# Performance work log

Measured on AMD Instinct MI355X. Metric: run time of the kernel, lower is better.

## Reference

```python
import jax, jax.numpy as jnp
import numpy as np

B, C, H, W = 32, 512, 32, 32
C8 = C // 8


def setup_inputs() -> dict:
    key = jax.random.key(0)
    ks = jax.random.split(key, 10)
    s = 1.0 / np.sqrt(C)
    return {
        "x": jax.random.normal(ks[0], (B, C, H, W), dtype=jnp.float32),
        "hha": jax.random.normal(ks[1], (B, C, H, W), dtype=jnp.float32),
        "wq": jax.random.normal(ks[2], (C8, C), dtype=jnp.float32) * s,
        "bq": jax.random.normal(ks[3], (C8,), dtype=jnp.float32) * 0.01,
        "wk": jax.random.normal(ks[4], (C8, C), dtype=jnp.float32) * s,
        "bk": jax.random.normal(ks[5], (C8,), dtype=jnp.float32) * 0.01,
        "wv": jax.random.normal(ks[6], (C, C), dtype=jnp.float32) * s,
        "bv": jax.random.normal(ks[7], (C,), dtype=jnp.float32) * 0.01,
        "gamma": jax.random.normal(ks[8], (1,), dtype=jnp.float32) * 0.5,
    }


def reference(x, hha, wq, bq, wk, bk, wv, bv, gamma):
    b, c, h, w = x.shape
    hw = h * w
    # 1x1 convs == per-pixel channel matmuls
    q = (jnp.einsum('bchw,oc->bohw', x, wq) + bq[None, :, None, None]).reshape(b, -1, hw)
    k = (jnp.einsum('bchw,oc->bohw', x, wk) + bk[None, :, None, None]).reshape(b, -1, hw)
    v = (jnp.einsum('bchw,oc->bohw', x, wv) + bv[None, :, None, None]).reshape(b, c, hw)
    # energy[b, i, j] = q[b, :, i] . k[b, :, j]  (no 1/sqrt(d) scaling, as in source)
    energy = jnp.einsum('bci,bcj->bij', q, k)          # [B, HW, HW]
    attention = jax.nn.softmax(energy, axis=-1)
    # out = V @ attention^T : out[b, c, i] = sum_j v[b, c, j] * attention[b, i, j]
    out = jnp.einsum('bcj,bij->bci', v, attention).reshape(b, c, h, w)
    rgb_out = gamma * out + x
    hha_out = gamma * out + hha
    return (attention, rgb_out, hha_out)
```

## Files before the change

### kernel.cpp

```cpp
#include <hip/hip_runtime.h>

#define B_N   32
#define C_N   512
#define HW_N  1024
#define C8_N  64

typedef short bf16x8 __attribute__((ext_vector_type(8)));
typedef float f32x4  __attribute__((ext_vector_type(4)));

static __device__ __forceinline__ unsigned int bf16_bits(float a)
{
    unsigned int u = __float_as_uint(a);
    return (u + 0x7fffu + ((u >> 16) & 1u)) >> 16;
}

static __device__ __forceinline__ unsigned int pack2_bf16(float a, float b)
{
    return bf16_bits(a) | (bf16_bits(b) << 16);
}

__global__ __launch_bounds__(256) void xsplit_transpose_kernel(
    const float* __restrict__ x, unsigned int* __restrict__ xt)
{
    const int b   = blockIdx.z;
    const int c0  = blockIdx.y * 64;
    const int p0  = blockIdx.x * 64;
    const int tid = threadIdx.x;

    __shared__ unsigned int Ls[64][65];

    const float* xb = x + ((size_t)b * C_N + c0) * HW_N + p0;
    {
        const int c = tid >> 4;
        const int p = (tid & 15) * 4;
        #pragma unroll
        for (int s = 0; s < 4; ++s) {
            const float4 t = *(const float4*)(xb + (size_t)(c + 16 * s) * HW_N + p);
            const float v[4] = { t.x, t.y, t.z, t.w };
            #pragma unroll
            for (int j = 0; j < 4; ++j) {
                const unsigned int hi = bf16_bits(v[j]);
                const float hif = __uint_as_float(hi << 16);
                const unsigned int lo = bf16_bits(v[j] - hif);
                Ls[c + 16 * s][p + j] = (hi << 16) | lo;
            }
        }
    }
    __syncthreads();
    unsigned int* xo = xt + ((size_t)b * HW_N + p0) * C_N + c0;
    {
        const int p = tid >> 4;
        const int c = (tid & 15) * 4;
        #pragma unroll
        for (int s = 0; s < 4; ++s) {
            uint4 r;
            r.x = Ls[c + 0][p + 16 * s];
            r.y = Ls[c + 1][p + 16 * s];
            r.z = Ls[c + 2][p + 16 * s];
            r.w = Ls[c + 3][p + 16 * s];
            *(uint4*)(xo + (size_t)(p + 16 * s) * C_N + c) = r;
        }
    }
}

__global__ __launch_bounds__(256) void qkv_mfma_kernel(
    const unsigned int* __restrict__ xt,
    const float* __restrict__ wq, const float* __restrict__ bq,
    const float* __restrict__ wk, const float* __restrict__ bk,
    const float* __restrict__ wv, const float* __restrict__ bv,
    float* __restrict__ qk, unsigned short* __restrict__ vout)
{
    const int b    = blockIdx.z;
    const int by   = blockIdx.y;
    const int p0   = blockIdx.x * 128;
    const int tid  = threadIdx.x;
    const bool qkblk = (by == 0);

    __shared__ __align__(16) unsigned short AsHi[128 * 64];
    __shared__ __align__(16) unsigned short AsLo[128 * 64];
    __shared__ __align__(16) unsigned short BsHi[128 * 64];
    __shared__ __align__(16) unsigned short BsLo[128 * 64];

    const int sq = tid & 7;
    const int sr = tid >> 3;

    const int lane = tid & 63;
    const int wave = tid >> 6;
    const int wrow = (wave >> 1) * 64;
    const int wcol = (wave & 1) * 64;
    const int lrow = lane & 15;
    const int lk   = lane >> 4;

    const unsigned int* bt = xt + ((size_t)b * HW_N + p0) * C_N;

    f32x4 acc[4][4] = {};
    float4 ra[4][2];
    uint4  rb[4][2];

    auto wrowptr = [&](int r) -> const float* {
        if (qkblk) return (r < 64) ? (wq + (size_t)r * C_N)
                                   : (wk + (size_t)(r - 64) * C_N);
        return wv + (size_t)((by - 1) * 128 + r) * C_N;
    };

    auto load_tiles = [&](int k0) {
        #pragma unroll
        for (int s = 0; s < 4; ++s) {
            const int r = sr + 32 * s;
            const float* pa = wrowptr(r) + k0 + sq * 8;
            ra[s][0] = *(const float4*)(pa);
            ra[s][1] = *(const float4*)(pa + 4);
            const unsigned int* pb = bt + (size_t)r * C_N + k0 + sq * 8;
            rb[s][0] = *(const uint4*)(pb);
            rb[s][1] = *(const uint4*)(pb + 4);
        }
    };

    auto write_tiles = [&]() {
        #pragma unroll
        for (int s = 0; s < 4; ++s) {
            const int r  = sr + 32 * s;
            const int ch = sq ^ (r & 7);
            const float e[8] = { ra[s][0].x, ra[s][0].y, ra[s][0].z, ra[s][0].w,
                                 ra[s][1].x, ra[s][1].y, ra[s][1].z, ra[s][1].w };
            unsigned int h[8];
            #pragma unroll
            for (int j = 0; j < 8; ++j) h[j] = bf16_bits(e[j]);
            uint4 ah;
            ah.x = h[0] | (h[1] << 16); ah.y = h[2] | (h[3] << 16);
            ah.z = h[4] | (h[5] << 16); ah.w = h[6] | (h[7] << 16);
            *reinterpret_cast<uint4*>(&AsHi[r * 64 + ch * 8]) = ah;
            if (qkblk) {
                unsigned int l[8];
                #pragma unroll
                for (int j = 0; j < 8; ++j) {
                    const float hf = __uint_as_float(h[j] << 16);
                    l[j] = bf16_bits(e[j] - hf);
                }
                uint4 al;
                al.x = l[0] | (l[1] << 16); al.y = l[2] | (l[3] << 16);
                al.z = l[4] | (l[5] << 16); al.w = l[6] | (l[7] << 16);
                *reinterpret_cast<uint4*>(&AsLo[r * 64 + ch * 8]) = al;
            }
            const unsigned int q0[8] = { rb[s][0].x, rb[s][0].y, rb[s][0].z, rb[s][0].w,
                                         rb[s][1].x, rb[s][1].y, rb[s][1].z, rb[s][1].w };
            uint4 bh, bl;
            bh.x = (q0[0] >> 16) | (q0[1] & 0xffff0000u);
            bh.y = (q0[2] >> 16) | (q0[3] & 0xffff0000u);
            bh.z = (q0[4] >> 16) | (q0[5] & 0xffff0000u);
            bh.w = (q0[6] >> 16) | (q0[7] & 0xffff0000u);
            bl.x = (q0[0] & 0xffffu) | (q0[1] << 16);
            bl.y = (q0[2] & 0xffffu) | (q0[3] << 16);
            bl.z = (q0[4] & 0xffffu) | (q0[5] << 16);
            bl.w = (q0[6] & 0xffffu) | (q0[7] << 16);
            *reinterpret_cast<uint4*>(&BsHi[r * 64 + ch * 8]) = bh;
            *reinterpret_cast<uint4*>(&BsLo[r * 64 + ch * 8]) = bl;
        }
    };

    load_tiles(0);
    for (int kt = 0; kt < C_N / 64; ++kt) {
        __syncthreads();
        write_tiles();
        __syncthreads();
        if (kt + 1 < C_N / 64) load_tiles((kt + 1) * 64);

        #pragma unroll
        for (int kb = 0; kb < 2; ++kb) {
            bf16x8 bfh[4], bfl[4];
            #pragma unroll
            for (int n = 0; n < 4; ++n) {
                const int r  = wcol + n * 16 + lrow;
                const int ch = (kb * 4 + lk) ^ (lrow & 7);
                bfh[n] = *reinterpret_cast<const bf16x8*>(&BsHi[r * 64 + ch * 8]);
                bfl[n] = *reinterpret_cast<const bf16x8*>(&BsLo[r * 64 + ch * 8]);
            }
            #pragma unroll
            for (int m = 0; m < 4; ++m) {
                const int r  = wrow + m * 16 + lrow;
                const int ch = (kb * 4 + lk) ^ (lrow & 7);
                const bf16x8 ah = *reinterpret_cast<const bf16x8*>(&AsHi[r * 64 + ch * 8]);
                #pragma unroll
                for (int n = 0; n < 4; ++n) {
                    acc[m][n] = __builtin_amdgcn_mfma_f32_16x16x32_bf16(ah, bfh[n], acc[m][n], 0, 0, 0);
                    acc[m][n] = __builtin_amdgcn_mfma_f32_16x16x32_bf16(ah, bfl[n], acc[m][n], 0, 0, 0);
                }
                if (qkblk) {
                    const bf16x8 al = *reinterpret_cast<const bf16x8*>(&AsLo[r * 64 + ch * 8]);
                    #pragma unroll
                    for (int n = 0; n < 4; ++n)
                        acc[m][n] = __builtin_amdgcn_mfma_f32_16x16x32_bf16(al, bfh[n], acc[m][n], 0, 0, 0);
                }
            }
        }
    }

    #pragma unroll
    for (int m = 0; m < 4; ++m) {
        #pragma unroll
        for (int rr = 0; rr < 4; ++rr) {
            const int r = wrow + m * 16 + lk * 4 + rr;
            if (qkblk) {
                const float bi = (r < 64) ? bq[r] : bk[r - 64];
                float* dst = qk + ((size_t)b * 128 + r) * HW_N + p0 + wcol + lrow;
                #pragma unroll
                for (int n = 0; n < 4; ++n)
                    dst[n * 16] = acc[m][n][rr] + bi;
            } else {
                const int vr = (by - 1) * 128 + r;
                const float bi = bv[vr];
                unsigned short* dst = vout + ((size_t)b * C_N + vr) * HW_N + p0 + wcol + lrow;
                #pragma unroll
                for (int n = 0; n < 4; ++n)
                    dst[n * 16] = (unsigned short)bf16_bits(acc[m][n][rr] + bi);
            }
        }
    }
}

__global__ __launch_bounds__(256) void qkt_transpose_kernel(
    const float* __restrict__ qk, unsigned int* __restrict__ qkT)
{
    const int b   = blockIdx.z;
    const int m0  = blockIdx.y * 64;
    const int p0  = blockIdx.x * 64;
    const int tid = threadIdx.x;

    __shared__ unsigned int Ls[64][65];

    const float* src = qk + ((size_t)b * 128 + m0) * HW_N + p0;
    {
        const int m = tid >> 4;
        const int p = (tid & 15) * 4;
        #pragma unroll
        for (int s = 0; s < 4; ++s) {
            const float4 t = *(const float4*)(src + (size_t)(m + 16 * s) * HW_N + p);
            const float v[4] = { t.x, t.y, t.z, t.w };
            #pragma unroll
            for (int j = 0; j < 4; ++j) {
                const unsigned int hi = bf16_bits(v[j]);
                const float hif = __uint_as_float(hi << 16);
                const unsigned int lo = bf16_bits(v[j] - hif);
                Ls[m + 16 * s][p + j] = (hi << 16) | lo;
            }
        }
    }
    __syncthreads();
    unsigned int* dst = qkT + ((size_t)b * HW_N + p0) * 128 + m0;
    {
        const int p = tid >> 4;
        const int m = (tid & 15) * 4;
        #pragma unroll
        for (int s = 0; s < 4; ++s) {
            uint4 r;
            r.x = Ls[m + 0][p + 16 * s];
            r.y = Ls[m + 1][p + 16 * s];
            r.z = Ls[m + 2][p + 16 * s];
            r.w = Ls[m + 3][p + 16 * s];
            *(uint4*)(dst + (size_t)(p + 16 * s) * 128 + m) = r;
        }
    }
}

__global__ __launch_bounds__(256) void energy_mfma_kernel(
    const unsigned int* __restrict__ qkT, float* __restrict__ att)
{
    const int b   = blockIdx.z;
    const int i0  = blockIdx.y * 128;
    const int j0  = blockIdx.x * 128;
    const int tid = threadIdx.x;

    __shared__ __align__(16) unsigned short AsHi[128 * 64];
    __shared__ __align__(16) unsigned short AsLo[128 * 64];
    __shared__ __align__(16) unsigned short BsHi[128 * 64];
    __shared__ __align__(16) unsigned short BsLo[128 * 64];

    const int sq = tid & 7;
    const int sr = tid >> 3;

    const int lane = tid & 63;
    const int wave = tid >> 6;
    const int wrow = (wave >> 1) * 64;
    const int wcol = (wave & 1) * 64;
    const int lrow = lane & 15;
    const int lk   = lane >> 4;

    #pragma unroll
    for (int s = 0; s < 4; ++s) {
        const int r  = sr + 32 * s;
        const int ch = sq ^ (r & 7);
        {
            const unsigned int* pa = qkT + ((size_t)b * HW_N + i0 + r) * 128 + sq * 8;
            const uint4 u0 = *(const uint4*)(pa);
            const uint4 u1 = *(const uint4*)(pa + 4);
            uint4 h, l;
            h.x = (u0.x >> 16) | (u0.y & 0xffff0000u);
            h.y = (u0.z >> 16) | (u0.w & 0xffff0000u);
            h.z = (u1.x >> 16) | (u1.y & 0xffff0000u);
            h.w = (u1.z >> 16) | (u1.w & 0xffff0000u);
            l.x = (u0.x & 0xffffu) | (u0.y << 16);
            l.y = (u0.z & 0xffffu) | (u0.w << 16);
            l.z = (u1.x & 0xffffu) | (u1.y << 16);
            l.w = (u1.z & 0xffffu) | (u1.w << 16);
            *reinterpret_cast<uint4*>(&AsHi[r * 64 + ch * 8]) = h;
            *reinterpret_cast<uint4*>(&AsLo[r * 64 + ch * 8]) = l;
        }
        {
            const unsigned int* pb = qkT + ((size_t)b * HW_N + j0 + r) * 128 + 64 + sq * 8;
            const uint4 u0 = *(const uint4*)(pb);
            const uint4 u1 = *(const uint4*)(pb + 4);
            uint4 h, l;
            h.x = (u0.x >> 16) | (u0.y & 0xffff0000u);
            h.y = (u0.z >> 16) | (u0.w & 0xffff0000u);
            h.z = (u1.x >> 16) | (u1.y & 0xffff0000u);
            h.w = (u1.z >> 16) | (u1.w & 0xffff0000u);
            l.x = (u0.x & 0xffffu) | (u0.y << 16);
            l.y = (u0.z & 0xffffu) | (u0.w << 16);
            l.z = (u1.x & 0xffffu) | (u1.y << 16);
            l.w = (u1.z & 0xffffu) | (u1.w << 16);
            *reinterpret_cast<uint4*>(&BsHi[r * 64 + ch * 8]) = h;
            *reinterpret_cast<uint4*>(&BsLo[r * 64 + ch * 8]) = l;
        }
    }
    __syncthreads();

    f32x4 acc[4][4] = {};
    #pragma unroll
    for (int kb = 0; kb < 2; ++kb) {
        bf16x8 bfh[4], bfl[4];
        #pragma unroll
        for (int n = 0; n < 4; ++n) {
            const int r  = wcol + n * 16 + lrow;
            const int ch = (kb * 4 + lk) ^ (lrow & 7);
            bfh[n] = *reinterpret_cast<const bf16x8*>(&BsHi[r * 64 + ch * 8]);
            bfl[n] = *reinterpret_cast<const bf16x8*>(&BsLo[r * 64 + ch * 8]);
        }
        #pragma unroll
        for (int m = 0; m < 4; ++m) {
            const int r  = wrow + m * 16 + lrow;
            const int ch = (kb * 4 + lk) ^ (lrow & 7);
            const bf16x8 ah = *reinterpret_cast<const bf16x8*>(&AsHi[r * 64 + ch * 8]);
            const bf16x8 al = *reinterpret_cast<const bf16x8*>(&AsLo[r * 64 + ch * 8]);
            #pragma unroll
            for (int n = 0; n < 4; ++n) {
                acc[m][n] = __builtin_amdgcn_mfma_f32_16x16x32_bf16(ah, bfh[n], acc[m][n], 0, 0, 0);
                acc[m][n] = __builtin_amdgcn_mfma_f32_16x16x32_bf16(ah, bfl[n], acc[m][n], 0, 0, 0);
                acc[m][n] = __builtin_amdgcn_mfma_f32_16x16x32_bf16(al, bfh[n], acc[m][n], 0, 0, 0);
            }
        }
    }

    #pragma unroll
    for (int m = 0; m < 4; ++m) {
        #pragma unroll
        for (int rr = 0; rr < 4; ++rr) {
            const int i = i0 + wrow + m * 16 + lk * 4 + rr;
            float* dst = att + ((size_t)b * HW_N + i) * HW_N + j0 + wcol + lrow;
            #pragma unroll
            for (int n = 0; n < 4; ++n)
                dst[n * 16] = acc[m][n][rr];
        }
    }
}

__global__ __launch_bounds__(256) void softmax_kernel(float* __restrict__ att)
{
    const size_t row = blockIdx.x;
    float* e = att + row * (size_t)HW_N;
    const int tid  = threadIdx.x;
    const int wv_  = tid >> 6;
    const int lane = tid & 63;

    float4 v = ((const float4*)e)[tid];

    float m = fmaxf(fmaxf(v.x, v.y), fmaxf(v.z, v.w));
    #pragma unroll
    for (int off = 32; off > 0; off >>= 1)
        m = fmaxf(m, __shfl_down(m, off, 64));
    __shared__ float red[4];
    if (lane == 0) red[wv_] = m;
    __syncthreads();
    m = fmaxf(fmaxf(red[0], red[1]), fmaxf(red[2], red[3]));
    __syncthreads();

    float4 ex;
    ex.x = __expf(v.x - m); ex.y = __expf(v.y - m);
    ex.z = __expf(v.z - m); ex.w = __expf(v.w - m);
    float s = ex.x + ex.y + ex.z + ex.w;
    #pragma unroll
    for (int off = 32; off > 0; off >>= 1)
        s += __shfl_down(s, off, 64);
    if (lane == 0) red[wv_] = s;
    __syncthreads();
    s = red[0] + red[1] + red[2] + red[3];

    const float inv = 1.0f / s;
    ex.x *= inv; ex.y *= inv; ex.z *= inv; ex.w *= inv;
    ((float4*)e)[tid] = ex;
}

__global__ __launch_bounds__(256) void out_kernel(
    const unsigned short* __restrict__ vout, const float* __restrict__ att,
    const float* __restrict__ x, const float* __restrict__ hha,
    const float* __restrict__ gamma,
    float* __restrict__ rgb, float* __restrict__ hho)
{
    const int b   = blockIdx.z;
    const int c0  = blockIdx.y * 128;
    const int i0  = blockIdx.x * 128;
    const int tid = threadIdx.x;

    const unsigned short* vptr = vout + (size_t)(b * C_N + c0) * HW_N;
    const float* aptr = att + (size_t)b * HW_N * HW_N + (size_t)i0 * HW_N;

    __shared__ __align__(16) unsigned short Vs[128 * 64];
    __shared__ __align__(16) unsigned short Ps[128 * 64];

    const int sq = tid & 7;
    const int sr = tid >> 3;

    const int lane = tid & 63;
    const int wave = tid >> 6;
    const int wrow = (wave >> 1) * 64;
    const int wcol = (wave & 1) * 64;
    const int lrow = lane & 15;
    const int lk   = lane >> 4;

    f32x4 acc[4][4] = {};
    uint4  ra[4];
    float4 rb[4][2];

    auto load_tiles = [&](int j0) {
        #pragma unroll
        for (int s = 0; s < 4; ++s) {
            ra[s] = *(const uint4*)(vptr + (size_t)(sr + 32 * s) * HW_N + j0 + sq * 8);
            const float* pb = aptr + (size_t)(sr + 32 * s) * HW_N + j0 + sq * 8;
            rb[s][0] = *(const float4*)(pb);
            rb[s][1] = *(const float4*)(pb + 4);
        }
    };

    auto write_tiles = [&]() {
        #pragma unroll
        for (int s = 0; s < 4; ++s) {
            const int r  = sr + 32 * s;
            const int ch = sq ^ (r & 7);
            *reinterpret_cast<uint4*>(&Vs[r * 64 + ch * 8]) = ra[s];
            uint4 wb;
            wb.x = pack2_bf16(rb[s][0].x, rb[s][0].y);
            wb.y = pack2_bf16(rb[s][0].z, rb[s][0].w);
            wb.z = pack2_bf16(rb[s][1].x, rb[s][1].y);
            wb.w = pack2_bf16(rb[s][1].z, rb[s][1].w);
            *reinterpret_cast<uint4*>(&Ps[r * 64 + ch * 8]) = wb;
        }
    };

    load_tiles(0);
    for (int jt = 0; jt < HW_N / 64; ++jt) {
        __syncthreads();
        write_tiles();
        __syncthreads();
        if (jt + 1 < HW_N / 64) load_tiles((jt + 1) * 64);

        #pragma unroll
        for (int kb = 0; kb < 2; ++kb) {
            bf16x8 af[4], bf[4];
            #pragma unroll
            for (int m = 0; m < 4; ++m) {
                const int r  = wrow + m * 16 + lrow;
                const int ch = (kb * 4 + lk) ^ (lrow & 7);
                af[m] = *reinterpret_cast<const bf16x8*>(&Vs[r * 64 + ch * 8]);
            }
            #pragma unroll
            for (int n = 0; n < 4; ++n) {
                const int r  = wcol + n * 16 + lrow;
                const int ch = (kb * 4 + lk) ^ (lrow & 7);
                bf[n] = *reinterpret_cast<const bf16x8*>(&Ps[r * 64 + ch * 8]);
            }
            #pragma unroll
            for (int m = 0; m < 4; ++m)
                #pragma unroll
                for (int n = 0; n < 4; ++n)
                    acc[m][n] = __builtin_amdgcn_mfma_f32_16x16x32_bf16(
                        af[m], bf[n], acc[m][n], 0, 0, 0);
        }
    }

    const float g    = gamma[0];
    const int   crow = c0 + wrow + lk * 4;
    const int   icol = i0 + wcol + lrow;
    #pragma unroll
    for (int m = 0; m < 4; ++m) {
        #pragma unroll
        for (int rr = 0; rr < 4; ++rr) {
            const int c = crow + m * 16 + rr;
            const size_t base = ((size_t)b * C_N + c) * HW_N + icol;
            #pragma unroll
            for (int n = 0; n < 4; ++n) {
                const float o  = acc[m][n][rr];
                const float xv = x[base + n * 16];
                const float hv = hha[base + n * 16];
                rgb[base + n * 16] = fmaf(g, o, xv);
                hho[base + n * 16] = fmaf(g, o, hv);
            }
        }
    }
}

extern "C" void kernel_launch(void* const* d_in, const int* in_sizes, int n_in,
                              void* d_out, int out_size, void* d_ws, size_t ws_size,
                              hipStream_t stream)
{
    const float* x     = (const float*)d_in[0];
    const float* hha   = (const float*)d_in[1];
    const float* wq    = (const float*)d_in[2];
    const float* bq    = (const float*)d_in[3];
    const float* wk    = (const float*)d_in[4];
    const float* bk    = (const float*)d_in[5];
    const float* wv    = (const float*)d_in[6];
    const float* bv    = (const float*)d_in[7];
    const float* gamma = (const float*)d_in[8];

    float* out = (float*)d_out;
    float* att = out;
    float* rgb = att + (size_t)B_N * HW_N * HW_N;
    float* hho = rgb + (size_t)B_N * C_N * HW_N;

    float*          qkbuf = (float*)d_ws;
    unsigned short* vbuf  = (unsigned short*)(qkbuf + (size_t)B_N * 128 * HW_N);
    unsigned int*   qkTb  = (unsigned int*)(vbuf + (size_t)B_N * C_N * HW_N);

    unsigned int* xt = (unsigned int*)att;

    xsplit_transpose_kernel<<<dim3(HW_N / 64, C_N / 64, B_N), 256, 0, stream>>>(x, xt);
    qkv_mfma_kernel<<<dim3(HW_N / 128, 5, B_N), 256, 0, stream>>>(
        xt, wq, bq, wk, bk, wv, bv, qkbuf, vbuf);
    qkt_transpose_kernel<<<dim3(HW_N / 64, 2, B_N), 256, 0, stream>>>(qkbuf, qkTb);
    energy_mfma_kernel<<<dim3(HW_N / 128, HW_N / 128, B_N), 256, 0, stream>>>(qkTb, att);
    softmax_kernel<<<dim3(B_N * HW_N), 256, 0, stream>>>(att);
    out_kernel<<<dim3(HW_N / 128, C_N / 128, B_N), 256, 0, stream>>>(
        vbuf, att, x, hha, gamma, rgb, hho);
}
```

Measured before the change: 678.0 us.

## Double-buffer global-load registers and use raw barriers in projection and PV GEMMs

Both the projection GEMM and the attention-times-V GEMM now keep two register sets of prefetched global tiles, so loads run two k-steps ahead instead of one. __syncthreads is replaced by an explicit lgkmcnt(0) wait plus s_barrier, which avoids the compiler's full vmcnt drain and keeps the outstanding global loads in flight across barriers. The cost is higher register pressure, which may lower occupancy or cause spills.

```diff
diff --git a/kernel.cpp b/kernel.cpp
--- a/kernel.cpp
+++ b/kernel.cpp
@@ -7,6 +7,8 @@
 
 typedef short bf16x8 __attribute__((ext_vector_type(8)));
 typedef float f32x4  __attribute__((ext_vector_type(4)));
+
+#define LGKM0() asm volatile("s_waitcnt lgkmcnt(0)" ::: "memory")
 
 static __device__ __forceinline__ unsigned int bf16_bits(float a)
 {
@@ -93,9 +95,9 @@
 
     const unsigned int* bt = xt + ((size_t)b * HW_N + p0) * C_N;
 
-    f32x4 acc[4][4] = {};
+    f32x4  acc[4][4] = {};
     float4 ra[4][2];
-    uint4  rb[4][2];
+    uint4  rb0[4][2], rb1[4][2];
 
     auto wrowptr = [&](int r) -> const float* {
         if (qkblk) return (r < 64) ? (wq + (size_t)r * C_N)
@@ -103,20 +105,24 @@
         return wv + (size_t)((by - 1) * 128 + r) * C_N;
     };
 
-    auto load_tiles = [&](int k0) {
-        #pragma unroll
-        for (int s = 0; s < 4; ++s) {
-            const int r = sr + 32 * s;
-            const float* pa = wrowptr(r) + k0 + sq * 8;
+    auto loadW = [&](int k0) {
+        #pragma unroll
+        for (int s = 0; s < 4; ++s) {
+            const float* pa = wrowptr(sr + 32 * s) + k0 + sq * 8;
             ra[s][0] = *(const float4*)(pa);
             ra[s][1] = *(const float4*)(pa + 4);
-            const unsigned int* pb = bt + (size_t)r * C_N + k0 + sq * 8;
+        }
+    };
+    auto loadX = [&](int k0, uint4 (&rb)[4][2]) {
+        #pragma unroll
+        for (int s = 0; s < 4; ++s) {
+            const unsigned int* pb = bt + (size_t)(sr + 32 * s) * C_N + k0 + sq * 8;
             rb[s][0] = *(const uint4*)(pb);
             rb[s][1] = *(const uint4*)(pb + 4);
         }
     };
 
-    auto write_tiles = [&]() {
+    auto write_tiles = [&](uint4 (&rb)[4][2]) {
         #pragma unroll
         for (int s = 0; s < 4; ++s) {
             const int r  = sr + 32 * s;
@@ -158,13 +164,7 @@
         }
     };
 
-    load_tiles(0);
-    for (int kt = 0; kt < C_N / 64; ++kt) {
-        __syncthreads();
-        write_tiles();
-        __syncthreads();
-        if (kt + 1 < C_N / 64) load_tiles((kt + 1) * 64);
-
+    auto compute = [&]() {
         #pragma unroll
         for (int kb = 0; kb < 2; ++kb) {
             bf16x8 bfh[4], bfl[4];
@@ -193,6 +193,27 @@
                 }
             }
         }
+    };
+
+    loadX(0, rb0);
+    loadX(64, rb1);
+    loadW(0);
+    for (int kt = 0; kt < 8; kt += 2) {
+        write_tiles(rb0);
+        LGKM0();
+        __builtin_amdgcn_s_barrier();
+        if (kt + 2 < 8) loadX((kt + 2) * 64, rb0);
+        loadW((kt + 1) * 64);
+        compute();
+        LGKM0();
+        __builtin_amdgcn_s_barrier();
+        write_tiles(rb1);
+        LGKM0();
+        __builtin_amdgcn_s_barrier();
+        if (kt + 3 < 8) { loadX((kt + 3) * 64, rb1); loadW((kt + 2) * 64); }
+        compute();
+        LGKM0();
+        __builtin_amdgcn_s_barrier();
     }
 
     #pragma unroll
@@ -426,11 +447,11 @@
     const int lrow = lane & 15;
     const int lk   = lane >> 4;
 
-    f32x4 acc[4][4] = {};
-    uint4  ra[4];
-    float4 rb[4][2];
-
-    auto load_tiles = [&](int j0) {
+    f32x4  acc[4][4] = {};
+    uint4  ra0[4], ra1[4];
+    float4 rb0[4][2], rb1[4][2];
+
+    auto load_set = [&](int j0, uint4 (&ra)[4], float4 (&rb)[4][2]) {
         #pragma unroll
         for (int s = 0; s < 4; ++s) {
             ra[s] = *(const uint4*)(vptr + (size_t)(sr + 32 * s) * HW_N + j0 + sq * 8);
@@ -440,7 +461,7 @@
         }
     };
 
-    auto write_tiles = [&]() {
+    auto write_set = [&](uint4 (&ra)[4], float4 (&rb)[4][2]) {
         #pragma unroll
         for (int s = 0; s < 4; ++s) {
             const int r  = sr + 32 * s;
@@ -455,13 +476,7 @@
         }
     };
 
-    load_tiles(0);
-    for (int jt = 0; jt < HW_N / 64; ++jt) {
-        __syncthreads();
-        write_tiles();
-        __syncthreads();
-        if (jt + 1 < HW_N / 64) load_tiles((jt + 1) * 64);
-
+    auto compute = [&]() {
         #pragma unroll
         for (int kb = 0; kb < 2; ++kb) {
             bf16x8 af[4], bf[4];
@@ -484,6 +499,25 @@
                     acc[m][n] = __builtin_amdgcn_mfma_f32_16x16x32_bf16(
                         af[m], bf[n], acc[m][n], 0, 0, 0);
         }
+    };
+
+    load_set(0, ra0, rb0);
+    load_set(64, ra1, rb1);
+    for (int jt = 0; jt < 16; jt += 2) {
+        write_set(ra0, rb0);
+        LGKM0();
+        __builtin_amdgcn_s_barrier();
+        if (jt + 2 < 16) load_set((jt + 2) * 64, ra0, rb0);
+        compute();
+        LGKM0();
+        __builtin_amdgcn_s_barrier();
+        write_set(ra1, rb1);
+        LGKM0();
+        __builtin_amdgcn_s_barrier();
+        if (jt + 3 < 16) load_set((jt + 3) * 64, ra1, rb1);
+        compute();
+        LGKM0();
+        __builtin_amdgcn_s_barrier();
     }
 
     const float g    = gamma[0];
```

New measurement: 695.0 us. +2.5%, slower.
